# Performance work log

Measured on AMD Instinct MI355X. Metric: run time of the kernel, lower is better.

## Reference

```python
import jax, jax.numpy as jnp
import numpy as np

MEM_DIM = 2000
FEA_DIM = 256
SHRINK_THRES = 0.0025
EPS = 1e-06


def setup_inputs() -> dict:
    key = jax.random.key(0)
    k1, k2 = jax.random.split(key)
    x = jax.random.normal(k1, (65536, FEA_DIM), dtype=jnp.float32)
    stdv = 1.0 / np.sqrt(FEA_DIM)
    weight = jax.random.uniform(k2, (MEM_DIM, FEA_DIM), dtype=jnp.float32,
                                minval=-stdv, maxval=stdv)
    temperature = jnp.asarray(0.5, dtype=jnp.float32)
    return {"input": x, "weight": weight, "temperature": temperature}


def hard_shrink_relu(a, lambd=SHRINK_THRES, epsilon=EPS):
    a = jnp.clip(a, -10.0, 10.0)
    denom = jnp.maximum(jnp.abs(a - lambd) + epsilon, epsilon)
    out = jax.nn.relu(a - lambd) * a / denom
    return jnp.where(jnp.isnan(out) | jnp.isinf(out), 0.0, out)


def reference(input, weight, temperature):
    mem_dim = weight.shape[0]
    inv_m = 1.0 / mem_dim
    x = jnp.clip(input, -10.0, 10.0)                      # [N, F]
    att = jnp.einsum('nf,mf->nm', x, weight)              # [N, M]
    att = jax.nn.softmax(att / temperature, axis=1)
    # shrink_thres > 0 branch
    att = hard_shrink_relu(att)
    weight_sum = jnp.sum(att, axis=1, keepdims=True)      # [N, 1]
    zero_mask = weight_sum < 1e-08
    att = att / (weight_sum + 1e-08)
    att = jnp.where(zero_mask, inv_m, att)                # rows with ~zero sum -> uniform
    att = jnp.where(jnp.isnan(att) | jnp.isinf(att), inv_m, att)
    output = jnp.einsum('nm,mf->nf', att, weight)         # [N, F]
    return output, att
```

## Files before the change

kernel.cpp:

```cpp
#include <hip/hip_runtime.h>
#include <hip/hip_bf16.h>
#include <cstdint>

#define N_ROWS 65536
#define FEA    256
#define MEM    2000
#define MEMP   2048
#define LAMBD  0.0025f
#define SEPS   1e-6f
#define NW     16
#define NTILE  2048
#define PGRID  256

typedef __attribute__((ext_vector_type(8))) _Float16 f16x8;
typedef __attribute__((ext_vector_type(8))) short    bf16x8;
typedef __attribute__((ext_vector_type(4))) float    f32x4;

__device__ __forceinline__ short f2bf(float f) {
    union { float f; uint32_t u; } v; v.f = f;
    uint32_t r = v.u + 0x7fffu + ((v.u >> 16) & 1u);
    return (short)(r >> 16);
}

__global__ __launch_bounds__(256) void prep_kernel(const float* __restrict__ W,
                                                   const float* __restrict__ temp,
                                                   _Float16* __restrict__ Whl2,
                                                   short* __restrict__ Wt) {
    __shared__ float tile[8][260];
    const int t  = threadIdx.x;
    const int m0 = blockIdx.x * 8;
    const int row = t >> 5, col = (t & 31) * 8;
    const int m = m0 + row;
    const float invT = 1.0f / temp[0];
    if (m < MEM) {
        f32x4 a = *(const f32x4*)(W + (size_t)m * FEA + col);
        f32x4 b = *(const f32x4*)(W + (size_t)m * FEA + col + 4);
        #pragma unroll
        for (int u = 0; u < 4; ++u) { tile[row][col+u] = a[u]; tile[row][col+4+u] = b[u]; }
    } else {
        #pragma unroll
        for (int u = 0; u < 8; ++u) tile[row][col+u] = 0.f;
    }
    __syncthreads();
    {
        const int c = col >> 5, q = (col >> 3) & 3;
        const int tt = m >> 4, lr = m & 15;
        _Float16 hi[8], lo[8];
        #pragma unroll
        for (int j = 0; j < 8; ++j) {
            float w = tile[row][col + j] * invT;
            _Float16 h = (_Float16)w;
            hi[j] = h;
            lo[j] = (_Float16)((w - (float)h) * 2048.0f);
        }
        _Float16* dst = Whl2 + (((size_t)(tt * 8 + c)) << 10) + (q * 16 + lr) * 16;
        *(f16x8*)dst       = *(f16x8*)&hi[0];
        *(f16x8*)(dst + 8) = *(f16x8*)&lo[0];
    }
    {
        short buf[8];
        #pragma unroll
        for (int j = 0; j < 8; ++j) buf[j] = f2bf(tile[j][t]);
        *(bf16x8*)(Wt + (size_t)t * MEMP + m0) = *(bf16x8*)&buf[0];
    }
}

__global__ __launch_bounds__(1024, 4) void score_kernel(const float* __restrict__ x,
                                                        const _Float16* __restrict__ Whl2,
                                                        float* __restrict__ att) {
    __shared__ __align__(16) _Float16 ah_s[32][264];
    __shared__ __align__(16) _Float16 al_s[32][264];
    __shared__ float redbuf[NW][32];
    __shared__ float redglob[32];

    const int tid  = threadIdx.x;
    const int lane = tid & 63;
    const int wid  = tid >> 6;
    const int lr   = lane & 15;
    const int q    = lane >> 4;
    const bool lastv = (wid < 13);
    const f32x4 z0 = (f32x4){0.f, 0.f, 0.f, 0.f};
    const float inv_m = 1.0f / (float)MEM;

    auto xred = [&](float v[2][4], bool ismax) {
        #pragma unroll
        for (int m = 1; m < 16; m <<= 1)
            #pragma unroll
            for (int rg = 0; rg < 2; ++rg)
                #pragma unroll
                for (int i = 0; i < 4; ++i) {
                    float o = __shfl_xor(v[rg][i], m, 64);
                    v[rg][i] = ismax ? fmaxf(v[rg][i], o) : (v[rg][i] + o);
                }
        if (lr == 0) {
            #pragma unroll
            for (int rg = 0; rg < 2; ++rg)
                #pragma unroll
                for (int i = 0; i < 4; ++i) redbuf[wid][rg * 16 + q * 4 + i] = v[rg][i];
        }
        __syncthreads();
        if (tid < 32) {
            float r = redbuf[0][tid];
            #pragma unroll
            for (int w = 1; w < NW; ++w) {
                float o = redbuf[w][tid];
                r = ismax ? fmaxf(r, o) : (r + o);
            }
            redglob[tid] = r;
        }
        __syncthreads();
        #pragma unroll
        for (int rg = 0; rg < 2; ++rg)
            #pragma unroll
            for (int i = 0; i < 4; ++i) v[rg][i] = redglob[rg * 16 + q * 4 + i];
        __syncthreads();
    };

    #pragma unroll 1
    for (int g = blockIdx.x; g < NTILE; g += PGRID) {
        const size_t r0 = (size_t)g * 32;

        {
            const int srow = tid >> 5, scol = (tid & 31) * 8;
            const float* xp = x + (r0 + srow) * FEA + scol;
            f32x4 v0 = *(const f32x4*)xp;
            f32x4 v1 = *(const f32x4*)(xp + 4);
            #pragma unroll
            for (int w = 0; w < 4; ++w) {
                float f0 = fminf(fmaxf(v0[w], -10.f), 10.f);
                float f1 = fminf(fmaxf(v1[w], -10.f), 10.f);
                _Float16 h0 = (_Float16)f0, h1 = (_Float16)f1;
                ah_s[srow][scol + w]     = h0;
                ah_s[srow][scol + 4 + w] = h1;
                al_s[srow][scol + w]     = (_Float16)((f0 - (float)h0) * 2048.0f);
                al_s[srow][scol + 4 + w] = (_Float16)((f1 - (float)h1) * 2048.0f);
            }
        }
        __syncthreads();

        f32x4 acc[2][8];
        #pragma unroll
        for (int rg = 0; rg < 2; ++rg)
            #pragma unroll
            for (int jj = 0; jj < 8; ++jj) acc[rg][jj] = z0;

        #pragma unroll 1
        for (int c = 0; c < 8; ++c) {
            f16x8 ah[2], al[2];
            #pragma unroll
            for (int rg = 0; rg < 2; ++rg) {
                ah[rg] = *(const f16x8*)&ah_s[rg * 16 + lr][c * 32 + q * 8];
                al[rg] = *(const f16x8*)&al_s[rg * 16 + lr][c * 32 + q * 8];
            }
            #pragma unroll
            for (int jj = 0; jj < 8; ++jj) {
                const int t = wid + 16 * jj;
                const _Float16* bp = Whl2 + (((size_t)(t * 8 + c)) << 10) + lane * 16;
                f16x8 bh = *(const f16x8*)bp;
                f16x8 bl = *(const f16x8*)(bp + 8);
                #pragma unroll
                for (int rg = 0; rg < 2; ++rg) {
                    f32x4 t1 = __builtin_amdgcn_mfma_f32_16x16x32_f16(al[rg], bh, z0, 0, 0, 0);
                    t1 = __builtin_amdgcn_mfma_f32_16x16x32_f16(ah[rg], bl, t1, 0, 0, 0);
                    acc[rg][jj] = __builtin_amdgcn_mfma_f32_16x16x32_f16(ah[rg], bh, acc[rg][jj], 0, 0, 0);
                    acc[rg][jj] += t1 * (1.0f / 2048.0f);
                }
            }
        }

        float M[2][4];
        #pragma unroll
        for (int rg = 0; rg < 2; ++rg)
            #pragma unroll
            for (int i = 0; i < 4; ++i) M[rg][i] = -3.0e38f;
        #pragma unroll
        for (int jj = 0; jj < 8; ++jj) {
            if (jj < 7 || lastv) {
                #pragma unroll
                for (int rg = 0; rg < 2; ++rg)
                    #pragma unroll
                    for (int i = 0; i < 4; ++i) M[rg][i] = fmaxf(M[rg][i], acc[rg][jj][i]);
            }
        }
        xred(M, true);

        #pragma unroll
        for (int jj = 0; jj < 8; ++jj) {
            const bool v = (jj < 7) || lastv;
            #pragma unroll
            for (int rg = 0; rg < 2; ++rg)
                #pragma unroll
                for (int i = 0; i < 4; ++i)
                    acc[rg][jj][i] = v ? __expf(acc[rg][jj][i] - M[rg][i]) : 0.0f;
        }

        float Z[2][4];
        #pragma unroll
        for (int rg = 0; rg < 2; ++rg)
            #pragma unroll
            for (int i = 0; i < 4; ++i) Z[rg][i] = 0.f;
        #pragma unroll
        for (int jj = 0; jj < 8; ++jj)
            #pragma unroll
            for (int rg = 0; rg < 2; ++rg)
                #pragma unroll
                for (int i = 0; i < 4; ++i) Z[rg][i] += acc[rg][jj][i];
        xred(Z, false);

        #pragma unroll
        for (int rg = 0; rg < 2; ++rg)
            #pragma unroll
            for (int i = 0; i < 4; ++i) Z[rg][i] = __builtin_amdgcn_rcpf(Z[rg][i]);
        #pragma unroll
        for (int jj = 0; jj < 8; ++jj)
            #pragma unroll
            for (int rg = 0; rg < 2; ++rg)
                #pragma unroll
                for (int i = 0; i < 4; ++i) {
                    float a = acc[rg][jj][i] * Z[rg][i];
                    float d = a - LAMBD;
                    float o = d * a * __builtin_amdgcn_rcpf(d + SEPS);
                    acc[rg][jj][i] = (d > 0.f) ? o : 0.f;
                }

        float WS[2][4];
        #pragma unroll
        for (int rg = 0; rg < 2; ++rg)
            #pragma unroll
            for (int i = 0; i < 4; ++i) WS[rg][i] = 0.f;
        #pragma unroll
        for (int jj = 0; jj < 8; ++jj)
            #pragma unroll
            for (int rg = 0; rg < 2; ++rg)
                #pragma unroll
                for (int i = 0; i < 4; ++i) WS[rg][i] += acc[rg][jj][i];
        xred(WS, false);

        float scl[2][4];
        bool  zr[2][4];
        #pragma unroll
        for (int rg = 0; rg < 2; ++rg)
            #pragma unroll
            for (int i = 0; i < 4; ++i) {
                scl[rg][i] = __builtin_amdgcn_rcpf(WS[rg][i] + 1e-8f);
                zr[rg][i]  = (WS[rg][i] < 1e-8f);
            }

        #pragma unroll
        for (int rg = 0; rg < 2; ++rg)
            #pragma unroll
            for (int i = 0; i < 4; ++i) {
                float* p = att + (r0 + rg * 16 + q * 4 + i) * (size_t)MEM + wid * 16 + lr;
                #pragma unroll
                for (int jj = 0; jj < 8; ++jj) {
                    if (jj < 7 || lastv) {
                        float vv = zr[rg][i] ? inv_m : acc[rg][jj][i] * scl[rg][i];
                        p[jj * 256] = vv;
                    }
                }
            }
    }
}

__global__ __launch_bounds__(512) void gemm2_kernel(const float* __restrict__ att,
                                                    const short* __restrict__ Wt,
                                                    float* __restrict__ out) {
    __shared__ short Asm[2][128][40];
    __shared__ short Bsm[2][256][40];
    const int tid  = threadIdx.x;
    const int lane = tid & 63;
    const int wid  = tid >> 6;
    const int rg   = wid >> 2;
    const int cg   = wid & 3;
    const int lr   = lane & 15;
    const int lk   = (lane >> 4) * 8;
    const size_t r0 = (size_t)blockIdx.x * 128;

    const int sa_row = tid >> 2, sa_ko = (tid & 3) * 8;
    const int sb_f   = tid >> 1, sb_ko = (tid & 1) * 16;

    auto stage = [&](int buf, int kc) {
        const int k0 = kc * 32;
        {
            int k = k0 + sa_ko;
            short b[8];
            if (k < MEM) {
                const float* ap = att + (r0 + sa_row) * (size_t)MEM + k;
                f32x4 v0 = *(const f32x4*)ap;
                f32x4 v1 = *(const f32x4*)(ap + 4);
                #pragma unroll
                for (int u = 0; u < 4; ++u) { b[u] = f2bf(v0[u]); b[4+u] = f2bf(v1[u]); }
            } else {
                #pragma unroll
                for (int u = 0; u < 8; ++u) b[u] = 0;
            }
            *(bf16x8*)&Asm[buf][sa_row][sa_ko] = *(bf16x8*)&b[0];
        }
        {
            const short* wp = Wt + (size_t)sb_f * MEMP + k0 + sb_ko;
            bf16x8 b0 = *(const bf16x8*)wp;
            bf16x8 b1 = *(const bf16x8*)(wp + 8);
            *(bf16x8*)&Bsm[buf][sb_f][sb_ko]     = b0;
            *(bf16x8*)&Bsm[buf][sb_f][sb_ko + 8] = b1;
        }
    };

    f32x4 acc[4][4];
    #pragma unroll
    for (int i = 0; i < 4; ++i)
        #pragma unroll
        for (int j = 0; j < 4; ++j) acc[i][j] = (f32x4){0.f, 0.f, 0.f, 0.f};

    stage(0, 0);
    int cur = 0;
    for (int kc = 0; kc < 63; ++kc) {
        __syncthreads();
        if (kc + 1 < 63) stage(cur ^ 1, kc + 1);
        bf16x8 a_[4], b_[4];
        #pragma unroll
        for (int i = 0; i < 4; ++i) a_[i] = *(const bf16x8*)&Asm[cur][rg * 64 + i * 16 + lr][lk];
        #pragma unroll
        for (int j = 0; j < 4; ++j) b_[j] = *(const bf16x8*)&Bsm[cur][cg * 64 + j * 16 + lr][lk];
        #pragma unroll
        for (int i = 0; i < 4; ++i)
            #pragma unroll
            for (int j = 0; j < 4; ++j)
                acc[i][j] = __builtin_amdgcn_mfma_f32_16x16x32_bf16(a_[i], b_[j], acc[i][j], 0, 0, 0);
        cur ^= 1;
    }

    #pragma unroll
    for (int i = 0; i < 4; ++i)
        #pragma unroll
        for (int j = 0; j < 4; ++j)
            #pragma unroll
            for (int ii = 0; ii < 4; ++ii) {
                size_t row = r0 + rg * 64 + i * 16 + (lane >> 4) * 4 + ii;
                out[row * FEA + cg * 64 + j * 16 + lr] = acc[i][j][ii];
            }
}

extern "C" void kernel_launch(void* const* d_in, const int* in_sizes, int n_in,
                              void* d_out, int out_size, void* d_ws, size_t ws_size,
                              hipStream_t stream) {
    const float* x = (const float*)d_in[0];
    const float* W = (const float*)d_in[1];
    const float* T = (const float*)d_in[2];
    float* out = (float*)d_out;
    float* att = out + (size_t)N_ROWS * FEA;
    _Float16* Whl2 = (_Float16*)d_ws;
    short*    Wt   = (short*)((char*)d_ws + (2u << 20));

    prep_kernel<<<dim3(256), dim3(256), 0, stream>>>(W, T, Whl2, Wt);
    score_kernel<<<dim3(PGRID), dim3(1024), 0, stream>>>(x, Whl2, att);
    gemm2_kernel<<<dim3(N_ROWS / 128), dim3(512), 0, stream>>>(att, Wt, out);
}
```

Before: 526.9 us.

## Fuse second GEMM into score kernel using LDS-resident bf16 attention tile

Removes the separate gemm2 kernel. The normalized attention tile for each 32-row block is now written as bf16 into shared memory, reusing the x staging buffers, and multiplied against the transposed weight directly with MFMA. This avoids re-reading the 512MB fp32 attention matrix from global memory. The cross-wave reduction also drops the single-thread final stage: every thread now reads all partials itself, which saves one barrier. The cost is extra serial MFMA work per block at low parallelism, with the B operand streamed from global/L2 without LDS staging, plus more LDS and sync pressure.

```diff
diff --git a/kernel.cpp b/kernel.cpp
--- a/kernel.cpp
+++ b/kernel.cpp
@@ -11,6 +11,7 @@
 #define NW     16
 #define NTILE  2048
 #define PGRID  256
+#define ALDS   2056
 
 typedef __attribute__((ext_vector_type(8))) _Float16 f16x8;
 typedef __attribute__((ext_vector_type(8))) short    bf16x8;
@@ -65,13 +66,16 @@
     }
 }
 
-__global__ __launch_bounds__(1024, 4) void score_kernel(const float* __restrict__ x,
+__global__ __launch_bounds__(1024, 4) void fused_kernel(const float* __restrict__ x,
                                                         const _Float16* __restrict__ Whl2,
-                                                        float* __restrict__ att) {
-    __shared__ __align__(16) _Float16 ah_s[32][264];
-    __shared__ __align__(16) _Float16 al_s[32][264];
+                                                        const short* __restrict__ Wt,
+                                                        float* __restrict__ att,
+                                                        float* __restrict__ out) {
+    __shared__ __align__(16) char smem[32 * ALDS * 2];
     __shared__ float redbuf[NW][32];
-    __shared__ float redglob[32];
+    _Float16 (*ah_s)[264]   = reinterpret_cast<_Float16(*)[264]>(smem);
+    _Float16 (*al_s)[264]   = reinterpret_cast<_Float16(*)[264]>(smem + 32 * 264 * 2);
+    short    (*att_lds)[ALDS] = reinterpret_cast<short(*)[ALDS]>(smem);
 
     const int tid  = threadIdx.x;
     const int lane = tid & 63;
@@ -99,26 +103,25 @@
                 for (int i = 0; i < 4; ++i) redbuf[wid][rg * 16 + q * 4 + i] = v[rg][i];
         }
         __syncthreads();
-        if (tid < 32) {
-            float r = redbuf[0][tid];
-            #pragma unroll
-            for (int w = 1; w < NW; ++w) {
-                float o = redbuf[w][tid];
-                r = ismax ? fmaxf(r, o) : (r + o);
-            }
-            redglob[tid] = r;
-        }
-        __syncthreads();
-        #pragma unroll
-        for (int rg = 0; rg < 2; ++rg)
-            #pragma unroll
-            for (int i = 0; i < 4; ++i) v[rg][i] = redglob[rg * 16 + q * 4 + i];
+        #pragma unroll
+        for (int rg = 0; rg < 2; ++rg)
+            #pragma unroll
+            for (int i = 0; i < 4; ++i) {
+                float r = redbuf[0][rg * 16 + q * 4 + i];
+                #pragma unroll
+                for (int w = 1; w < NW; ++w) {
+                    float o = redbuf[w][rg * 16 + q * 4 + i];
+                    r = ismax ? fmaxf(r, o) : (r + o);
+                }
+                v[rg][i] = r;
+            }
         __syncthreads();
     };
 
     #pragma unroll 1
     for (int g = blockIdx.x; g < NTILE; g += PGRID) {
         const size_t r0 = (size_t)g * 32;
+        __syncthreads();
 
         {
             const int srow = tid >> 5, scol = (tid & 31) * 8;
@@ -246,98 +249,44 @@
                 zr[rg][i]  = (WS[rg][i] < 1e-8f);
             }
 
+        if (tid < 768) {
+            const int zrow = tid / 24, zc = tid % 24;
+            ((uint32_t*)&att_lds[zrow][2000])[zc] = 0u;
+        }
+
         #pragma unroll
         for (int rg = 0; rg < 2; ++rg)
             #pragma unroll
             for (int i = 0; i < 4; ++i) {
-                float* p = att + (r0 + rg * 16 + q * 4 + i) * (size_t)MEM + wid * 16 + lr;
+                const int arow = rg * 16 + q * 4 + i;
+                float* p = att + (r0 + arow) * (size_t)MEM + wid * 16 + lr;
                 #pragma unroll
                 for (int jj = 0; jj < 8; ++jj) {
                     if (jj < 7 || lastv) {
                         float vv = zr[rg][i] ? inv_m : acc[rg][jj][i] * scl[rg][i];
                         p[jj * 256] = vv;
+                        att_lds[arow][jj * 256 + wid * 16 + lr] = f2bf(vv);
                     }
                 }
             }
+        __syncthreads();
+
+        f32x4 acc2[2] = {z0, z0};
+        const short* wtp = Wt + (size_t)(wid * 16 + lr) * MEMP + q * 8;
+        #pragma unroll 3
+        for (int kc = 0; kc < 63; ++kc) {
+            bf16x8 a0 = *(const bf16x8*)&att_lds[lr]     [kc * 32 + q * 8];
+            bf16x8 a1 = *(const bf16x8*)&att_lds[16 + lr][kc * 32 + q * 8];
+            bf16x8 b  = *(const bf16x8*)(wtp + kc * 32);
+            acc2[0] = __builtin_amdgcn_mfma_f32_16x16x32_bf16(a0, b, acc2[0], 0, 0, 0);
+            acc2[1] = __builtin_amdgcn_mfma_f32_16x16x32_bf16(a1, b, acc2[1], 0, 0, 0);
+        }
+        #pragma unroll
+        for (int rg = 0; rg < 2; ++rg)
+            #pragma unroll
+            for (int i = 0; i < 4; ++i)
+                out[(r0 + rg * 16 + q * 4 + i) * FEA + wid * 16 + lr] = acc2[rg][i];
     }
-}
-
-__global__ __launch_bounds__(512) void gemm2_kernel(const float* __restrict__ att,
-                                                    const short* __restrict__ Wt,
-                                                    float* __restrict__ out) {
-    __shared__ short Asm[2][128][40];
-    __shared__ short Bsm[2][256][40];
-    const int tid  = threadIdx.x;
-    const int lane = tid & 63;
-    const int wid  = tid >> 6;
-    const int rg   = wid >> 2;
-    const int cg   = wid & 3;
-    const int lr   = lane & 15;
-    const int lk   = (lane >> 4) * 8;
-    const size_t r0 = (size_t)blockIdx.x * 128;
-
-    const int sa_row = tid >> 2, sa_ko = (tid & 3) * 8;
-    const int sb_f   = tid >> 1, sb_ko = (tid & 1) * 16;
-
-    auto stage = [&](int buf, int kc) {
-        const int k0 = kc * 32;
-        {
-            int k = k0 + sa_ko;
-            short b[8];
-            if (k < MEM) {
-                const float* ap = att + (r0 + sa_row) * (size_t)MEM + k;
-                f32x4 v0 = *(const f32x4*)ap;
-                f32x4 v1 = *(const f32x4*)(ap + 4);
-                #pragma unroll
-                for (int u = 0; u < 4; ++u) { b[u] = f2bf(v0[u]); b[4+u] = f2bf(v1[u]); }
-            } else {
-                #pragma unroll
-                for (int u = 0; u < 8; ++u) b[u] = 0;
-            }
-            *(bf16x8*)&Asm[buf][sa_row][sa_ko] = *(bf16x8*)&b[0];
-        }
-        {
-            const short* wp = Wt + (size_t)sb_f * MEMP + k0 + sb_ko;
-            bf16x8 b0 = *(const bf16x8*)wp;
-            bf16x8 b1 = *(const bf16x8*)(wp + 8);
-            *(bf16x8*)&Bsm[buf][sb_f][sb_ko]     = b0;
-            *(bf16x8*)&Bsm[buf][sb_f][sb_ko + 8] = b1;
-        }
-    };
-
-    f32x4 acc[4][4];
-    #pragma unroll
-    for (int i = 0; i < 4; ++i)
-        #pragma unroll
-        for (int j = 0; j < 4; ++j) acc[i][j] = (f32x4){0.f, 0.f, 0.f, 0.f};
-
-    stage(0, 0);
-    int cur = 0;
-    for (int kc = 0; kc < 63; ++kc) {
-        __syncthreads();
-        if (kc + 1 < 63) stage(cur ^ 1, kc + 1);
-        bf16x8 a_[4], b_[4];
-        #pragma unroll
-        for (int i = 0; i < 4; ++i) a_[i] = *(const bf16x8*)&Asm[cur][rg * 64 + i * 16 + lr][lk];
-        #pragma unroll
-        for (int j = 0; j < 4; ++j) b_[j] = *(const bf16x8*)&Bsm[cur][cg * 64 + j * 16 + lr][lk];
-        #pragma unroll
-        for (int i = 0; i < 4; ++i)
-            #pragma unroll
-            for (int j = 0; j < 4; ++j)
-                acc[i][j] = __builtin_amdgcn_mfma_f32_16x16x32_bf16(a_[i], b_[j], acc[i][j], 0, 0, 0);
-        cur ^= 1;
-    }
-
-    #pragma unroll
-    for (int i = 0; i < 4; ++i)
-        #pragma unroll
-        for (int j = 0; j < 4; ++j)
-            #pragma unroll
-            for (int ii = 0; ii < 4; ++ii) {
-                size_t row = r0 + rg * 64 + i * 16 + (lane >> 4) * 4 + ii;
-                out[row * FEA + cg * 64 + j * 16 + lr] = acc[i][j][ii];
-            }
 }
 
 extern "C" void kernel_launch(void* const* d_in, const int* in_sizes, int n_in,
@@ -352,6 +301,5 @@
     short*    Wt   = (short*)((char*)d_ws + (2u << 20));
 
     prep_kernel<<<dim3(256), dim3(256), 0, stream>>>(W, T, Whl2, Wt);
-    score_kernel<<<dim3(PGRID), dim3(1024), 0, stream>>>(x, Whl2, att);
-    gemm2_kernel<<<dim3(N_ROWS / 128), dim3(512), 0, stream>>>(att, Wt, out);
+    fused_kernel<<<dim3(PGRID), dim3(1024), 0, stream>>>(x, Whl2, Wt, att, out);
 }
```

Result: slower. 817.2 us (+55.1%).
